# Kernel tuning notes

Hardware: AMD Instinct MI355X
Metric: run time of the kernel (lower is better)

The kernel has to match this reference:

```python
import math
import jax, jax.numpy as jnp
import numpy as np

NUM_HEADS = 32
HIDDEN = 4096
HEAD_DIM = HIDDEN // NUM_HEADS  # 128
NEG_INF = -1e30


def _alibi_slopes(n: int) -> jnp.ndarray:
    cp2 = 2 ** math.floor(math.log2(n))
    base = 2.0 ** (-(2.0 ** (-(math.log2(cp2) - 3))))
    slopes = base ** np.arange(1, cp2 + 1, dtype=np.float64)
    if cp2 != n:
        extra_base = 2.0 ** (-(2.0 ** (-(math.log2(2 * cp2) - 3))))
        rem = min(cp2, n - cp2)
        extra = extra_base ** np.arange(1, 1 + 2 * rem, 2, dtype=np.float64)
        slopes = np.concatenate([slopes, extra])
    return jnp.asarray(slopes, dtype=jnp.float32)


def setup_inputs() -> dict:
    key = jax.random.key(0)
    k1, k2, k3 = jax.random.split(key, 3)
    B, S = 2, 2048
    hidden_states = jax.random.normal(k1, (B, S, HIDDEN), dtype=jnp.float32)
    Wqkv = jax.random.normal(k2, (HIDDEN, NUM_HEADS * HEAD_DIM + 2 * HEAD_DIM), dtype=jnp.float32) * 0.02
    Wo = jax.random.normal(k3, (HIDDEN, HIDDEN), dtype=jnp.float32) * 0.02
    return {"hidden_states": hidden_states, "Wqkv": Wqkv, "Wo": Wo}


def reference(hidden_states, Wqkv, Wo):
    B, S, H = hidden_states.shape
    nH, d = NUM_HEADS, HEAD_DIM
    scale = d ** -0.5

    qkv = hidden_states @ Wqkv                      # [B,S,nH*d + 2d]
    q = qkv[..., : nH * d].reshape(B, S, nH, d)     # [B,S,nH,d]
    k = qkv[..., nH * d: nH * d + d]                # [B,S,d] (single kv head, MQA)
    v = qkv[..., nH * d + d:]                       # [B,S,d]

    scores = jnp.einsum("bqhd,bkd->bhqk", q, k) * scale  # [B,nH,S,S]

    pos_q = jnp.arange(S)[:, None]
    pos_k = jnp.arange(S)[None, :]
    slopes = _alibi_slopes(nH)                       # [nH]
    alibi = slopes[:, None, None] * (pos_k - pos_q).astype(jnp.float32)  # [nH,S,S]
    causal = pos_k <= pos_q                          # [S,S]

    scores = jnp.where(causal[None, None], scores + alibi[None], NEG_INF)
    probs = jax.nn.softmax(scores, axis=-1)
    attn = jnp.einsum("bhqk,bkd->bqhd", probs, v).reshape(B, S, H)
    return attn @ Wo
```

## Files before the change

kernel.cpp:

```cpp
#include <hip/hip_runtime.h>
#include <hip/hip_bf16.h>

typedef __attribute__((ext_vector_type(8))) short bf16x8;
typedef __attribute__((ext_vector_type(4))) float f32x4;
typedef __attribute__((ext_vector_type(8))) unsigned short u16x8;
typedef __attribute__((ext_vector_type(4))) unsigned short u16x4;
typedef __attribute__((address_space(3))) const char* lds_cp;

__device__ __forceinline__ unsigned short f2bf(float x) {
    union { float f; unsigned u; } v; v.f = x;
    unsigned r = v.u + 0x7fff + ((v.u >> 16) & 1);
    return (unsigned short)(r >> 16);
}

__device__ __forceinline__ unsigned short f2bf_hw(float x) {
    __hip_bfloat16 h = __float2bfloat16(x);
    return *reinterpret_cast<unsigned short*>(&h);
}

__device__ __forceinline__ void gload16(const void* g, void* l) {
    __builtin_amdgcn_global_load_lds(
        (const __attribute__((address_space(1))) void*)g,
        (__attribute__((address_space(3))) void*)l, 16, 0, 0);
}

__device__ __forceinline__ bf16x8 ds128(lds_cp a) {
    bf16x8 r;
    asm volatile("ds_read_b128 %0, %1" : "=&v"(r) : "v"(a));
    return r;
}

__global__ __launch_bounds__(256) void cast_bf16_kernel(
    const float* __restrict__ src, unsigned short* __restrict__ dst, int n8) {
    int i = blockIdx.x * 256 + threadIdx.x;
    if (i >= n8) return;
    const float4* s = (const float4*)src + (size_t)i * 2;
    float4 a = s[0], b = s[1];
    u16x8 o;
    o[0] = f2bf(a.x); o[1] = f2bf(a.y); o[2] = f2bf(a.z); o[3] = f2bf(a.w);
    o[4] = f2bf(b.x); o[5] = f2bf(b.y); o[6] = f2bf(b.z); o[7] = f2bf(b.w);
    *(u16x8*)(dst + (size_t)i * 8) = o;
}

__global__ __launch_bounds__(256) void transpose_cast_kernel(
    const float* __restrict__ src, unsigned short* __restrict__ dst, int R, int C) {
    __shared__ float tile[32][33];
    const int bx = blockIdx.x * 32, by = blockIdx.y * 32;
    const int tx = threadIdx.x & 31, ty = threadIdx.x >> 5;
#pragma unroll
    for (int i = 0; i < 32; i += 8)
        tile[ty + i][tx] = src[(size_t)(by + ty + i) * C + (bx + tx)];
    __syncthreads();
#pragma unroll
    for (int i = 0; i < 32; i += 8)
        dst[(size_t)(bx + ty + i) * R + (by + tx)] = f2bf(tile[tx][ty + i]);
}

template <int OUTBF>
__global__ __launch_bounds__(256) void gemm_kernel(
    const unsigned short* __restrict__ A, const unsigned short* __restrict__ BT,
    void* __restrict__ Cp, int M, int N, int K) {
    __shared__ unsigned short Al[2][128 * 32];
    __shared__ unsigned short Bl[2][128 * 32];
    const int t = threadIdx.x;
    const int wid = t >> 6, lane = t & 63;
    const int l15 = lane & 15, lg = lane >> 4;
    const int bm = blockIdx.y * 128, bn = blockIdx.x * 128;
    const int wm = (wid >> 1) * 64, wn = (wid & 1) * 64;

    f32x4 acc[4][4];
#pragma unroll
    for (int i = 0; i < 4; ++i)
#pragma unroll
        for (int j = 0; j < 4; ++j) acc[i][j] = (f32x4)(0.f);

    const int nk = K >> 5;
    const int c0 = t, c1 = t + 256;

    auto stage = [&](int buf, int kt) {
        const unsigned short* Ab = A + (size_t)bm * K + kt * 32;
        const unsigned short* Bb = BT + (size_t)bn * K + kt * 32;
        gload16(Ab + (size_t)(c0 >> 2) * K + (c0 & 3) * 8, &Al[buf][wid * 64 * 8]);
        gload16(Ab + (size_t)(c1 >> 2) * K + (c1 & 3) * 8, &Al[buf][(256 + wid * 64) * 8]);
        gload16(Bb + (size_t)(c0 >> 2) * K + (c0 & 3) * 8, &Bl[buf][wid * 64 * 8]);
        gload16(Bb + (size_t)(c1 >> 2) * K + (c1 & 3) * 8, &Bl[buf][(256 + wid * 64) * 8]);
    };

    stage(0, 0);
    __syncthreads();
    for (int kt = 0; kt < nk; ++kt) {
        const int cur = kt & 1;
        if (kt + 1 < nk) stage(cur ^ 1, kt + 1);
        bf16x8 af[4], bfr[4];
#pragma unroll
        for (int i = 0; i < 4; ++i) {
            af[i]  = *(const bf16x8*)&Al[cur][(wm + i * 16 + l15) * 32 + lg * 8];
            bfr[i] = *(const bf16x8*)&Bl[cur][(wn + i * 16 + l15) * 32 + lg * 8];
        }
#pragma unroll
        for (int i = 0; i < 4; ++i)
#pragma unroll
            for (int j = 0; j < 4; ++j)
                acc[i][j] = __builtin_amdgcn_mfma_f32_16x16x32_bf16(af[i], bfr[j], acc[i][j], 0, 0, 0);
        __syncthreads();
    }

#pragma unroll
    for (int i = 0; i < 4; ++i)
#pragma unroll
        for (int j = 0; j < 4; ++j)
#pragma unroll
            for (int r = 0; r < 4; ++r) {
                const int row = bm + wm + i * 16 + lg * 4 + r;
                const int col = bn + wn + j * 16 + l15;
                if (OUTBF) ((unsigned short*)Cp)[(size_t)row * N + col] = f2bf(acc[i][j][r]);
                else       ((float*)Cp)[(size_t)row * N + col] = acc[i][j][r];
            }
}

#define SYNC1() do { __builtin_amdgcn_s_barrier(); \
    asm volatile("s_waitcnt lgkmcnt(0)" ::: "memory"); \
    __builtin_amdgcn_sched_barrier(0); } while (0)
#define GATE4() do { asm volatile("s_waitcnt vmcnt(4)" ::: "memory"); \
    __builtin_amdgcn_s_barrier(); __builtin_amdgcn_sched_barrier(0); } while (0)

template <int OUTBF>
__global__ __launch_bounds__(512, 2) void gemm256_kernel(
    const unsigned short* __restrict__ A, const unsigned short* __restrict__ BT,
    void* __restrict__ Cp, int K, int N) {
    __shared__ __align__(16) char lds[131072];
    const int t = threadIdx.x;
    const int wid = t >> 6, lane = t & 63;
    const int l15 = lane & 15, lg = lane >> 4;
    const int xcd = blockIdx.x & 7, idx = blockIdx.x >> 3;
    const int bm = ((xcd >> 1) * 4 + (idx >> 3)) * 256;
    const int bn = ((xcd & 1) * 8 + (idx & 7)) * 256;
    const int wmh = wid >> 2;
    const int wq  = wid & 3;
    const int bhf = wq >> 1;
    const int br0 = (wq & 1) * 64;

    auto Ab = [&](int b, int h) -> char* { return lds + ((b * 2 + h) << 14); };
    auto Bb = [&](int b, int h) -> char* { return lds + 65536 + ((b * 2 + h) << 14); };

    auto stage = [&](char* halfBase, const unsigned short* mat, int rowBase, int kt) {
#pragma unroll
        for (int j = 0; j < 2; ++j) {
            const int dbase = ((j << 3) + wid) << 10;
            const int d = dbase + lane * 16;
            const int r = d >> 7;
            const int c2 = (d ^ ((r & 7) << 4)) & 127;
            gload16(mat + (size_t)(rowBase + r) * K + (kt << 6) + (c2 >> 1),
                    halfBase + dbase);
        }
    };

    f32x4 acc[8][4];
#pragma unroll
    for (int i = 0; i < 8; ++i)
#pragma unroll
        for (int j = 0; j < 4; ++j) acc[i][j] = (f32x4)(0.f);

    bf16x8 afq[4][2];
    bf16x8 b0[2][2], b1[2][2];

    auto ldAq = [&](int b, int mh) {
        lds_cp base = (lds_cp)Ab(b, wmh);
#pragma unroll
        for (int i = 0; i < 4; ++i) {
            const int r = mh * 64 + i * 16 + l15;
            const int sw = (r & 7) << 4;
#pragma unroll
            for (int kk = 0; kk < 2; ++kk)
                afq[i][kk] = ds128(base + r * 128 + ((kk * 64 + lg * 16) ^ sw));
        }
    };
    auto ldBq = [&](bf16x8 (&bq)[2][2], int b, int nh) {
        lds_cp base = (lds_cp)Bb(b, bhf);
#pragma unroll
        for (int i = 0; i < 2; ++i) {
            const int r = br0 + (nh * 2 + i) * 16 + l15;
            const int sw = (r & 7) << 4;
#pragma unroll
            for (int kk = 0; kk < 2; ++kk)
                bq[i][kk] = ds128(base + r * 128 + ((kk * 64 + lg * 16) ^ sw));
        }
    };
    auto MFq = [&](int mh, int nh, bf16x8 (&bq)[2][2]) {
        __builtin_amdgcn_s_setprio(1);
#pragma unroll
        for (int i = 0; i < 4; ++i)
#pragma unroll
            for (int j = 0; j < 2; ++j)
#pragma unroll
                for (int kk = 0; kk < 2; ++kk)
                    acc[mh * 4 + i][nh * 2 + j] = __builtin_amdgcn_mfma_f32_16x16x32_bf16(
                        afq[i][kk], bq[j][kk], acc[mh * 4 + i][nh * 2 + j], 0, 0, 0);
        __builtin_amdgcn_s_setprio(0);
    };

    stage(Ab(0, 0), A, bm, 0);
    stage(Ab(0, 1), A, bm + 128, 0);
    stage(Bb(0, 0), BT, bn, 0);
    stage(Bb(0, 1), BT, bn + 128, 0);
    stage(Bb(1, 0), BT, bn, 1);
    stage(Bb(1, 1), BT, bn + 128, 1);
    asm volatile("s_waitcnt vmcnt(4)" ::: "memory");
    __builtin_amdgcn_s_barrier();
    __builtin_amdgcn_sched_barrier(0);

    const int kmask = (K >> 6) - 1;
    const int niter = K >> 7;
    for (int it = 0; it < niter; ++it) {
        const int kto = 2 * it + 1;
        const int kne = (2 * it + 2) & kmask;
        const int kno = (2 * it + 3) & kmask;
        ldAq(0, 0); ldBq(b0, 0, 0);
        stage(Ab(1, 0), A, bm, kto);
        SYNC1(); MFq(0, 0, b0); __builtin_amdgcn_s_barrier();
        ldBq(b1, 0, 1);
        stage(Ab(1, 1), A, bm + 128, kto);
        SYNC1(); MFq(0, 1, b1); __builtin_amdgcn_s_barrier();
        ldAq(0, 1);
        stage(Bb(0, 0), BT, bn, kne);
        SYNC1(); MFq(1, 1, b1); __builtin_amdgcn_s_barrier();
        stage(Bb(0, 1), BT, bn + 128, kne);
        SYNC1(); MFq(1, 0, b0); GATE4();
        ldAq(1, 0); ldBq(b0, 1, 0);
        stage(Ab(0, 0), A, bm, kne);
        SYNC1(); MFq(0, 0, b0); __builtin_amdgcn_s_barrier();
        ldBq(b1, 1, 1);
        stage(Ab(0, 1), A, bm + 128, kne);
        SYNC1(); MFq(0, 1, b1); __builtin_amdgcn_s_barrier();
        ldAq(1, 1);
        stage(Bb(1, 0), BT, bn, kno);
        SYNC1(); MFq(1, 1, b1); __builtin_amdgcn_s_barrier();
        stage(Bb(1, 1), BT, bn + 128, kno);
        SYNC1(); MFq(1, 0, b0); GATE4();
    }

#pragma unroll
    for (int mi = 0; mi < 8; ++mi)
#pragma unroll
        for (int ni = 0; ni < 4; ++ni)
#pragma unroll
            for (int rr = 0; rr < 4; ++rr) {
                const size_t off = (size_t)(bm + wmh * 128 + mi * 16 + lg * 4 + rr) * N +
                                   bn + wq * 64 + ni * 16 + l15;
                if (OUTBF) ((unsigned short*)Cp)[off] = f2bf(acc[mi][ni][rr]);
                else       ((float*)Cp)[off] = acc[mi][ni][rr];
            }
}

__global__ __launch_bounds__(256, 4) void attn_kernel(
    const unsigned short* __restrict__ qkv, unsigned short* __restrict__ attn, int S) {
    constexpr int LD = 4352;
    __shared__ unsigned short Kl[64 * 128];
    __shared__ unsigned short Vt[128 * 64];
    __shared__ unsigned short Pl[4][16 * 64];
    const int t = threadIdx.x, wid = t >> 6;
    const int lane = t & 63, l15 = lane & 15, lg = lane >> 4;
    const int h = blockIdx.y, b = blockIdx.z;
    const size_t rb = (size_t)b * S;
    const int nQB = S >> 6;
    const float scale2 = 0.08838834764831845f * 1.4426950408889634f;
    const float slope2 = exp2f(-0.25f * (float)(h + 1)) * 1.4426950408889634f;
    const float sr1 = slope2, sr2 = slope2 * 2.f, sr3 = slope2 * 3.f;

    for (int half = 0; half < 2; ++half) {
        const int qblk = half ? (nQB - 1 - (int)blockIdx.x) : (int)blockIdx.x;
        const int q0w = qblk * 64 + wid * 16;
        const int qlane = q0w + l15;
        const float aq = slope2 * (float)qlane;

        bf16x8 qf[4];
        {
            const unsigned short* qrow = qkv + (rb + qlane) * LD + h * 128 + lg * 8;
#pragma unroll
            for (int j = 0; j < 4; ++j) qf[j] = *(const bf16x8*)(qrow + j * 32);
        }
        f32x4 o[8];
#pragma unroll
        for (int i = 0; i < 8; ++i) o[i] = (f32x4)(0.f);
        float m_ = -1e30f, l_ = 0.f;

        const int ntile = qblk + 1;
        for (int tile = 0; tile < ntile; ++tile) {
            const int t0 = tile * 64;
            {
                const char* kbase = (const char*)(qkv + (rb + t0) * LD + 4096);
#pragma unroll
                for (int i = 0; i < 4; ++i) {
                    const int c = i * 256 + t;
                    const int krow = c >> 4;
                    gload16(kbase + (size_t)krow * (LD * 2) + (((c & 15) * 16) ^ ((krow & 7) << 4)),
                            (char*)Kl + (i * 256 + wid * 64) * 16);
                }
            }
            {
                const unsigned short* vs = qkv + (rb + t0 + lane) * LD + 4224 + wid * 32;
                u16x8 v0 = *(const u16x8*)vs;
                u16x8 v1 = *(const u16x8*)(vs + 8);
                u16x8 v2 = *(const u16x8*)(vs + 16);
                u16x8 v3 = *(const u16x8*)(vs + 24);
                const int kb = 2 * lane;
#pragma unroll
                for (int e = 0; e < 8; ++e) {
                    int dd = wid * 32 + e;
                    *(unsigned short*)((char*)Vt + dd * 128 + (kb ^ ((dd & 7) << 4))) = v0[e];
                    dd += 8;
                    *(unsigned short*)((char*)Vt + dd * 128 + (kb ^ ((dd & 7) << 4))) = v1[e];
                    dd += 8;
                    *(unsigned short*)((char*)Vt + dd * 128 + (kb ^ ((dd & 7) << 4))) = v2[e];
                    dd += 8;
                    *(unsigned short*)((char*)Vt + dd * 128 + (kb ^ ((dd & 7) << 4))) = v3[e];
                }
            }
            __syncthreads();

            f32x4 s4[4];
#pragma unroll
            for (int ct = 0; ct < 4; ++ct) {
                s4[ct] = (f32x4)(0.f);
                const int row = ct * 16 + l15;
                const int swz = (row & 7) << 4;
#pragma unroll
                for (int j = 0; j < 4; ++j) {
                    bf16x8 kf = *(const bf16x8*)((const char*)Kl + row * 256 +
                                                 ((j * 64 + lg * 16) ^ swz));
                    s4[ct] = __builtin_amdgcn_mfma_f32_16x16x32_bf16(kf, qf[j], s4[ct], 0, 0, 0);
                }
            }

            const float base = slope2 * (float)(t0 + lg * 4) - aq;
            float p4[4][4];
            float mx = -1e30f;
            const bool lastt = (tile == ntile - 1);
            const int dbase = t0 + lg * 4 - qlane;
#pragma unroll
            for (int ct = 0; ct < 4; ++ct) {
                const float bbc = base + slope2 * 16.f * (float)ct;
#pragma unroll
                for (int r = 0; r < 4; ++r) {
                    float sc = fmaf(s4[ct][r], scale2,
                                    bbc + (r == 0 ? 0.f : (r == 1 ? sr1 : (r == 2 ? sr2 : sr3))));
                    if (lastt && (dbase + ct * 16 + r > 0)) sc = -1e30f;
                    p4[ct][r] = sc;
                    mx = fmaxf(mx, sc);
                }
            }
            mx = fmaxf(mx, __shfl_xor(mx, 16));
            mx = fmaxf(mx, __shfl_xor(mx, 32));

            if (!__all(mx <= m_ + 8.0f)) {
                const float mnew = fmaxf(m_, mx);
                const float corr = exp2f(m_ - mnew);
                m_ = mnew;
                l_ *= corr;
                float cr[4];
#pragma unroll
                for (int r = 0; r < 4; ++r) cr[r] = __shfl(corr, lg * 4 + r);
#pragma unroll
                for (int n = 0; n < 8; ++n) {
                    o[n][0] *= cr[0]; o[n][1] *= cr[1];
                    o[n][2] *= cr[2]; o[n][3] *= cr[3];
                }
            }

            float rs = 0.f;
#pragma unroll
            for (int ct = 0; ct < 4; ++ct)
#pragma unroll
                for (int r = 0; r < 4; ++r) {
                    const float pv = exp2f(p4[ct][r] - m_);
                    p4[ct][r] = pv;
                    rs += pv;
                }
            rs += __shfl_xor(rs, 16);
            rs += __shfl_xor(rs, 32);
            l_ += rs;

            {
                char* pb = (char*)&Pl[wid][0] + l15 * 128;
                const int swz = (l15 & 7) << 4;
#pragma unroll
                for (int ct = 0; ct < 4; ++ct) {
                    u16x4 w;
                    w[0] = f2bf_hw(p4[ct][0]); w[1] = f2bf_hw(p4[ct][1]);
                    w[2] = f2bf_hw(p4[ct][2]); w[3] = f2bf_hw(p4[ct][3]);
                    *(u16x4*)(pb + ((ct * 32 + lg * 8) ^ swz)) = w;
                }
            }

            const char* pb = (const char*)&Pl[wid][0] + l15 * 128;
            const int pswz = (l15 & 7) << 4;
            bf16x8 pa0 = *(const bf16x8*)(pb + ((lg * 16) ^ pswz));
            bf16x8 pa1 = *(const bf16x8*)(pb + ((64 + lg * 16) ^ pswz));
#pragma unroll
            for (int n = 0; n < 8; ++n) {
                const int dd = n * 16 + l15;
                const int vswz = (dd & 7) << 4;
                bf16x8 vf0 = *(const bf16x8*)((const char*)Vt + dd * 128 + ((lg * 16) ^ vswz));
                bf16x8 vf1 = *(const bf16x8*)((const char*)Vt + dd * 128 + ((64 + lg * 16) ^ vswz));
                f32x4 a4 = __builtin_amdgcn_mfma_f32_16x16x32_bf16(pa0, vf0, o[n], 0, 0, 0);
                o[n] = __builtin_amdgcn_mfma_f32_16x16x32_bf16(pa1, vf1, a4, 0, 0, 0);
            }
            __syncthreads();
        }

        const float rl = 1.f / l_;
        float rv[4];
#pragma unroll
        for (int r = 0; r < 4; ++r) rv[r] = __shfl(rl, lg * 4 + r);
#pragma unroll
        for (int n = 0; n < 8; ++n)
#pragma unroll
            for (int r = 0; r < 4; ++r) {
                const int q = q0w + lg * 4 + r;
                attn[(rb + q) * 4096 + h * 128 + n * 16 + l15] = f2bf(o[n][r] * rv[r]);
            }
    }
}

extern "C" void kernel_launch(void* const* d_in, const int* in_sizes, int n_in,
                              void* d_out, int out_size, void* d_ws, size_t ws_size,
                              hipStream_t stream) {
    const float* hidden = (const float*)d_in[0];
    const float* Wqkv   = (const float*)d_in[1];
    const float* Wo     = (const float*)d_in[2];
    float* out = (float*)d_out;
    char* ws = (char*)d_ws;

    const int B = 2, S = 2048, H = 4096, NQ = 4352;
    const int M = B * S;

    unsigned short* hb  = (unsigned short*)(ws);
    unsigned short* wT  = (unsigned short*)(ws + 33554432);
    unsigned short* qkv = (unsigned short*)(ws + 33554432 + 35651584);

    cast_bf16_kernel<<<(M * H / 8) / 256, 256, 0, stream>>>(hidden, hb, M * H / 8);
    transpose_cast_kernel<<<dim3(NQ / 32, H / 32), 256, 0, stream>>>(Wqkv, wT, H, NQ);
    gemm_kernel<1><<<dim3(NQ / 128, M / 128), 256, 0, stream>>>(hb, wT, qkv, M, NQ, H);
    transpose_cast_kernel<<<dim3(H / 32, H / 32), 256, 0, stream>>>(Wo, wT, H, H);
    attn_kernel<<<dim3(16, 32, 2), 256, 0, stream>>>(qkv, hb, S);
    gemm256_kernel<0><<<dim3(256), 512, 0, stream>>>(hb, wT, out, H, H);
}
```

Baseline: 523.3 us.

## Double-buffer A fragments and prefetch LDS reads ahead of MFMA phases in GEMM

Splits the A register fragments into two sets so the next LDS fragment loads are issued one phase ahead of the MFMAs that use them. Full lgkmcnt(0) waits become partial counts, so part of the LDS read latency can overlap the matrix math. It also raises wave priority around the attention kernel's MFMA loops. The extra fragment registers raise VGPR pressure in a kernel already bounded at 512 threads and 2 blocks, and the partial wait counts must exactly match how many LDS reads are in flight.

```diff
diff --git a/kernel.cpp b/kernel.cpp
--- a/kernel.cpp
+++ b/kernel.cpp
@@ -118,11 +118,11 @@
             }
 }
 
-#define SYNC1() do { __builtin_amdgcn_s_barrier(); \
-    asm volatile("s_waitcnt lgkmcnt(0)" ::: "memory"); \
-    __builtin_amdgcn_sched_barrier(0); } while (0)
 #define GATE4() do { asm volatile("s_waitcnt vmcnt(4)" ::: "memory"); \
     __builtin_amdgcn_s_barrier(); __builtin_amdgcn_sched_barrier(0); } while (0)
+#define WAITL(N) do { __builtin_amdgcn_s_barrier(); \
+    asm volatile("s_waitcnt lgkmcnt(" #N ")" ::: "memory"); \
+    __builtin_amdgcn_sched_barrier(0); } while (0)
 
 template <int OUTBF>
 __global__ __launch_bounds__(512, 2) void gemm256_kernel(
@@ -161,10 +161,10 @@
 #pragma unroll
         for (int j = 0; j < 4; ++j) acc[i][j] = (f32x4)(0.f);
 
-    bf16x8 afq[4][2];
+    bf16x8 afA[4][2], afB[4][2];
     bf16x8 b0[2][2], b1[2][2];
 
-    auto ldAq = [&](int b, int mh) {
+    auto ldAq = [&](bf16x8 (&dst)[4][2], int b, int mh) {
         lds_cp base = (lds_cp)Ab(b, wmh);
 #pragma unroll
         for (int i = 0; i < 4; ++i) {
@@ -172,10 +172,10 @@
             const int sw = (r & 7) << 4;
 #pragma unroll
             for (int kk = 0; kk < 2; ++kk)
-                afq[i][kk] = ds128(base + r * 128 + ((kk * 64 + lg * 16) ^ sw));
+                dst[i][kk] = ds128(base + r * 128 + ((kk * 64 + lg * 16) ^ sw));
         }
     };
-    auto ldBq = [&](bf16x8 (&bq)[2][2], int b, int nh) {
+    auto ldBq = [&](bf16x8 (&dst)[2][2], int b, int nh) {
         lds_cp base = (lds_cp)Bb(b, bhf);
 #pragma unroll
         for (int i = 0; i < 2; ++i) {
@@ -183,10 +183,10 @@
             const int sw = (r & 7) << 4;
 #pragma unroll
             for (int kk = 0; kk < 2; ++kk)
-                bq[i][kk] = ds128(base + r * 128 + ((kk * 64 + lg * 16) ^ sw));
+                dst[i][kk] = ds128(base + r * 128 + ((kk * 64 + lg * 16) ^ sw));
         }
     };
-    auto MFq = [&](int mh, int nh, bf16x8 (&bq)[2][2]) {
+    auto MFq = [&](bf16x8 (&aq)[4][2], bf16x8 (&bq)[2][2], int mh, int nh) {
         __builtin_amdgcn_s_setprio(1);
 #pragma unroll
         for (int i = 0; i < 4; ++i)
@@ -195,7 +195,7 @@
 #pragma unroll
                 for (int kk = 0; kk < 2; ++kk)
                     acc[mh * 4 + i][nh * 2 + j] = __builtin_amdgcn_mfma_f32_16x16x32_bf16(
-                        afq[i][kk], bq[j][kk], acc[mh * 4 + i][nh * 2 + j], 0, 0, 0);
+                        aq[i][kk], bq[j][kk], acc[mh * 4 + i][nh * 2 + j], 0, 0, 0);
         __builtin_amdgcn_s_setprio(0);
     };
 
@@ -208,6 +208,7 @@
     asm volatile("s_waitcnt vmcnt(4)" ::: "memory");
     __builtin_amdgcn_s_barrier();
     __builtin_amdgcn_sched_barrier(0);
+    ldAq(afA, 0, 0); ldBq(b0, 0, 0);
 
     const int kmask = (K >> 6) - 1;
     const int niter = K >> 7;
@@ -215,28 +216,46 @@
         const int kto = 2 * it + 1;
         const int kne = (2 * it + 2) & kmask;
         const int kno = (2 * it + 3) & kmask;
-        ldAq(0, 0); ldBq(b0, 0, 0);
+        ldBq(b1, 0, 1);
         stage(Ab(1, 0), A, bm, kto);
-        SYNC1(); MFq(0, 0, b0); __builtin_amdgcn_s_barrier();
-        ldBq(b1, 0, 1);
+        WAITL(4);
+        MFq(afA, b0, 0, 0);
+        __builtin_amdgcn_s_barrier();
+        ldAq(afB, 0, 1);
         stage(Ab(1, 1), A, bm + 128, kto);
-        SYNC1(); MFq(0, 1, b1); __builtin_amdgcn_s_barrier();
-        ldAq(0, 1);
+        WAITL(8);
+        MFq(afA, b1, 0, 1);
+        __builtin_amdgcn_s_barrier();
         stage(Bb(0, 0), BT, bn, kne);
-        SYNC1(); MFq(1, 1, b1); __builtin_amdgcn_s_barrier();
+        WAITL(0);
+        MFq(afB, b1, 1, 1);
+        __builtin_amdgcn_s_barrier();
         stage(Bb(0, 1), BT, bn + 128, kne);
-        SYNC1(); MFq(1, 0, b0); GATE4();
-        ldAq(1, 0); ldBq(b0, 1, 0);
+        __builtin_amdgcn_s_barrier();
+        __builtin_amdgcn_sched_barrier(0);
+        MFq(afB, b0, 1, 0);
+        GATE4();
+        ldAq(afA, 1, 0); ldBq(b0, 1, 0);
+        ldBq(b1, 1, 1);
         stage(Ab(0, 0), A, bm, kne);
-        SYNC1(); MFq(0, 0, b0); __builtin_amdgcn_s_barrier();
-        ldBq(b1, 1, 1);
+        WAITL(4);
+        MFq(afA, b0, 0, 0);
+        __builtin_amdgcn_s_barrier();
+        ldAq(afB, 1, 1);
         stage(Ab(0, 1), A, bm + 128, kne);
-        SYNC1(); MFq(0, 1, b1); __builtin_amdgcn_s_barrier();
-        ldAq(1, 1);
+        WAITL(8);
+        MFq(afA, b1, 0, 1);
+        __builtin_amdgcn_s_barrier();
         stage(Bb(1, 0), BT, bn, kno);
-        SYNC1(); MFq(1, 1, b1); __builtin_amdgcn_s_barrier();
+        WAITL(0);
+        MFq(afB, b1, 1, 1);
+        __builtin_amdgcn_s_barrier();
         stage(Bb(1, 1), BT, bn + 128, kno);
-        SYNC1(); MFq(1, 0, b0); GATE4();
+        __builtin_amdgcn_s_barrier();
+        __builtin_amdgcn_sched_barrier(0);
+        MFq(afB, b0, 1, 0);
+        GATE4();
+        ldAq(afA, 0, 0); ldBq(b0, 0, 0);
     }
 
 #pragma unroll
@@ -319,6 +338,7 @@
             __syncthreads();
 
             f32x4 s4[4];
+            __builtin_amdgcn_s_setprio(1);
 #pragma unroll
             for (int ct = 0; ct < 4; ++ct) {
                 s4[ct] = (f32x4)(0.f);
@@ -331,6 +351,7 @@
                     s4[ct] = __builtin_amdgcn_mfma_f32_16x16x32_bf16(kf, qf[j], s4[ct], 0, 0, 0);
                 }
             }
+            __builtin_amdgcn_s_setprio(0);
 
             const float base = slope2 * (float)(t0 + lg * 4) - aq;
             float p4[4][4];
@@ -396,6 +417,7 @@
             const int pswz = (l15 & 7) << 4;
             bf16x8 pa0 = *(const bf16x8*)(pb + ((lg * 16) ^ pswz));
             bf16x8 pa1 = *(const bf16x8*)(pb + ((64 + lg * 16) ^ pswz));
+            __builtin_amdgcn_s_setprio(1);
 #pragma unroll
             for (int n = 0; n < 8; ++n) {
                 const int dd = n * 16 + l15;
@@ -405,6 +427,7 @@
                 f32x4 a4 = __builtin_amdgcn_mfma_f32_16x16x32_bf16(pa0, vf0, o[n], 0, 0, 0);
                 o[n] = __builtin_amdgcn_mfma_f32_16x16x32_bf16(pa1, vf1, a4, 0, 0, 0);
             }
+            __builtin_amdgcn_s_setprio(0);
             __syncthreads();
         }
 
```

Measured after the change: 588.6 us. +12.5%, slower.
